# Performance work log

Hardware: AMD Instinct MI355X
Metric: run time of the kernel (lower is better)

The kernel has to match this reference:

```python
import jax, jax.numpy as jnp
import numpy as np
import itertools

# hyperparameters (match init_kwargs cfg)
V_SIZE = 32000; D = 768; H = 12; NL = 2
K_BITS = 4; L_TAB = 4; M_COPIES = 2; HID = 3072
DK = D // H; R = 1 << K_BITS; EPS = 1e-6; RMS_EPS = 1e-5

def _protos_T():
    # corners of the {-1,+1}^K hypercube, transposed -> [K, R]
    corners = np.array(list(itertools.product([-1.0, 1.0], repeat=K_BITS)), dtype=np.float32)
    return jnp.asarray(corners.T)

def setup_inputs() -> dict:
    key = jax.random.key(0)
    ks = jax.random.split(key, 14)
    s = 0.02
    return {
        "in_idx": jax.random.randint(ks[0], (1, 1024), 0, V_SIZE),
        "tok_emb": jax.random.normal(ks[1], (V_SIZE, D), jnp.float32) * s,
        "norm1_w": jnp.ones((NL, D), jnp.float32),
        "qw": jax.random.normal(ks[2], (NL, D, D), jnp.float32) * s,
        "kw": jax.random.normal(ks[3], (NL, D, D), jnp.float32) * s,
        "vw": jax.random.normal(ks[4], (NL, D, D), jnp.float32) * s,
        "ow": jax.random.normal(ks[5], (NL, D, D), jnp.float32) * s,
        "ob": jnp.zeros((NL, D), jnp.float32),
        "norm2_w": jnp.ones((NL, D), jnp.float32),
        "ff_w1": jax.random.normal(ks[6], (NL, D, HID), jnp.float32) * s,
        "ff_w2": jax.random.normal(ks[7], (NL, D, HID), jnp.float32) * s,
        "ff_w3": jax.random.normal(ks[8], (NL, HID, D), jnp.float32) * s,
        "final_norm_w": jnp.ones((D,), jnp.float32),
        "out_w": jax.random.normal(ks[9], (D, V_SIZE), jnp.float32) * s,
        "planes_T": jax.random.normal(ks[10], (NL, M_COPIES, DK, L_TAB * K_BITS), jnp.float32),
    }

def _rmsnorm(x, w):
    return x * jax.lax.rsqrt(jnp.mean(x * x, axis=-1, keepdims=True) + RMS_EPS) * w

def _race_attention(h, qw, kw, vw, ow, ob, planes, protos_T):
    B, T, _ = h.shape
    Q = (h @ qw).reshape(B, T, H, DK)
    Kt = (h @ kw).reshape(B, T, H, DK)
    Vt = (h @ vw).reshape(B, T, H, DK)
    # RoPE (split-even/odd, concat halves variant, start position 0)
    theta = 10000.0 ** (-jnp.arange(0, DK, 2, dtype=jnp.float32) / DK)
    freq = jnp.arange(T, dtype=jnp.float32)[:, None] * theta[None, :]  # [T, DK/2]
    sin = jnp.sin(freq)[None, :, None, :]
    cos = jnp.cos(freq)[None, :, None, :]
    def rope(z):
        e, o = z[..., ::2], z[..., 1::2]
        return jnp.concatenate([e * cos - o * sin, e * sin + o * cos], axis=-1)
    Q, Kt = rope(Q), rope(Kt)
    to_hb = lambda z: jnp.transpose(z, (0, 2, 1, 3)).reshape(B * H, T, DK)
    Qh, Kh, Vh = to_hb(Q), to_hb(Kt), to_hb(Vt)
    N = M_COPIES * B * H
    scale = jnp.sqrt(jnp.float32(DK))
    # random-plane projections per model copy m: [M, BH, T, L*K]
    projK = jnp.einsum('ntd,mds->mnts', Kh, planes).reshape(N, T, L_TAB, K_BITS)
    projQ = jnp.einsum('ntd,mds->mnts', Qh, planes).reshape(N, T, L_TAB, K_BITS)
    probsK = jax.nn.softmax((jnp.tanh(projK) / scale) @ protos_T, axis=-1)  # [N,T,L,R]
    probsQ = jax.nn.softmax((jnp.tanh(projQ) / scale) @ protos_T, axis=-1)
    Vn = jnp.broadcast_to(Vh[None], (M_COPIES, B * H, T, DK)).reshape(N, T, DK)
    # causal prefix sums over time
    A_pref = jnp.cumsum(probsK, axis=1)                                     # [N,T,L,R]
    B_pref = jnp.cumsum(probsK[..., None] * Vn[:, :, None, None, :], axis=1)  # [N,T,L,R,DK]
    E_pref = B_pref / (A_pref[..., None] + EPS)
    out2 = jnp.einsum('ntlr,ntlrd->ntd', probsQ, E_pref)                    # [N,T,DK]
    out_h = out2.reshape(M_COPIES, B, H, T, DK).transpose(0, 1, 3, 2, 4)    # [M,B,T,H,DK]
    m = out_h.mean(axis=0)                                                  # [B,T,H,DK]
    # faithful to the source: permute to [B,H,T,DK] then row-major reshape to [B,T,H*DK]
    out = jnp.transpose(m, (0, 2, 1, 3)).reshape(B, T, H * DK)
    return out @ ow + ob

def reference(in_idx, tok_emb, norm1_w, qw, kw, vw, ow, ob, norm2_w,
              ff_w1, ff_w2, ff_w3, final_norm_w, out_w, planes_T):
    protos_T = _protos_T()
    x = tok_emb[in_idx]  # [B,T,D]
    for l in range(NL):
        h = _rmsnorm(x, norm1_w[l])
        x = x + _race_attention(h, qw[l], kw[l], vw[l], ow[l], ob[l], planes_T[l], protos_T)
        h = _rmsnorm(x, norm2_w[l])
        x = x + (jax.nn.silu(h @ ff_w1[l]) * (h @ ff_w2[l])) @ ff_w3[l]
    x = _rmsnorm(x, final_norm_w)
    return x @ out_w  # logits [B,T,V]
```

## Files before the change

### kernel.cpp

```cpp
#include <hip/hip_runtime.h>
#include <hip/hip_bf16.h>

#define T_SEQ 1024
#define D_MODEL 768
#define QKVW 2304
#define NHEAD 12
#define NLAYER 2
#define MCOPY 2
#define HID_DIM 3072
#define VSIZE 32000
#define NCH 32
#define TL 32

typedef __attribute__((ext_vector_type(8))) short short8;
typedef __attribute__((ext_vector_type(4))) float f32x4;

__device__ __forceinline__ short f2bf(float f) {
  unsigned u = __builtin_bit_cast(unsigned, f);
  u = (u + 0x7FFFu + ((u >> 16) & 1u)) >> 16;
  return (short)u;
}

__global__ __launch_bounds__(64) void stc_k(float* __restrict__ stc) {
  int t = blockIdx.x;
  int i = threadIdx.x;
  if (i < 32) {
    float theta = powf(10000.0f, -(float)i / 32.0f);
    float s, c;
    sincosf((float)t * theta, &s, &c);
    stc[t * 64 + 2 * i] = c;
    stc[t * 64 + 2 * i + 1] = s;
  }
}

__global__ __launch_bounds__(256) void embed_k(const int* __restrict__ idx,
                                               const float* __restrict__ emb,
                                               float* __restrict__ x) {
  int t = blockIdx.x;
  int r = idx[t];
  for (int d = threadIdx.x; d < D_MODEL; d += 256)
    x[t * D_MODEL + d] = emb[r * D_MODEL + d];
}

__global__ __launch_bounds__(256) void add_norm_k(float* __restrict__ x,
                                                  const float* __restrict__ parts,
                                                  int nparts,
                                                  const float* __restrict__ bias,
                                                  const float* __restrict__ w,
                                                  short* __restrict__ out) {
  int t = blockIdx.x, tid = threadIdx.x;
  float v[3];
  float ss = 0.f;
  #pragma unroll
  for (int j = 0; j < 3; ++j) {
    int i = tid + j * 256;
    float val = x[(size_t)t * D_MODEL + i];
    if (bias) val += bias[i];
    for (int p = 0; p < nparts; ++p)
      val += parts[(size_t)p * (T_SEQ * D_MODEL) + (size_t)t * D_MODEL + i];
    v[j] = val;
    ss += val * val;
  }
  __shared__ float red[256];
  red[tid] = ss; __syncthreads();
  for (int s = 128; s > 0; s >>= 1) {
    if (tid < s) red[tid] += red[tid + s];
    __syncthreads();
  }
  float inv = rsqrtf(red[0] / (float)D_MODEL + 1e-5f);
  #pragma unroll
  for (int j = 0; j < 3; ++j) {
    int i = tid + j * 256;
    if (nparts || bias) x[(size_t)t * D_MODEL + i] = v[j];
    out[(size_t)t * D_MODEL + i] = f2bf(v[j] * inv * w[i]);
  }
}

__device__ __forceinline__ void tr_tile(const float* __restrict__ W,
                                        short* __restrict__ WT, int K, int N,
                                        int n0, int k0, int tx, int ty) {
  __shared__ float tile[32][33];
  #pragma unroll
  for (int i = 0; i < 4; ++i)
    tile[ty + 8 * i][tx] = W[(size_t)(k0 + ty + 8 * i) * N + n0 + tx];
  __syncthreads();
  #pragma unroll
  for (int i = 0; i < 4; ++i)
    WT[(size_t)(n0 + ty + 8 * i) * K + k0 + tx] = f2bf(tile[tx][ty + 8 * i]);
}

#define SQ_W  ((size_t)D_MODEL * D_MODEL)
#define FF_W  ((size_t)D_MODEL * HID_DIM)
#define LAYER_W (4 * SQ_W + 3 * FF_W)

__global__ __launch_bounds__(256) void transpose_sq8(const float* __restrict__ qw,
                                                     const float* __restrict__ kw,
                                                     const float* __restrict__ vw,
                                                     const float* __restrict__ ow,
                                                     short* __restrict__ WB) {
  int z = blockIdx.z, layer = z >> 2, which = z & 3;
  const float* W = (which == 0) ? qw : (which == 1) ? kw : (which == 2) ? vw : ow;
  W += (size_t)layer * SQ_W;
  short* WT = WB + (size_t)layer * LAYER_W + (size_t)which * SQ_W;
  tr_tile(W, WT, D_MODEL, D_MODEL, blockIdx.x * 32, blockIdx.y * 32,
          threadIdx.x, threadIdx.y);
}

__global__ __launch_bounds__(256) void transpose_ff12(const float* __restrict__ W1g,
                                                      const float* __restrict__ W2g,
                                                      short* __restrict__ WB) {
  __shared__ float tile[32][33];
  int layer = blockIdx.z;
  const float* W1 = W1g + (size_t)layer * FF_W;
  const float* W2 = W2g + (size_t)layer * FF_W;
  short* WT = WB + (size_t)layer * LAYER_W + 4 * SQ_W;
  int tx = threadIdx.x, ty = threadIdx.y;
  int n0 = blockIdx.x * 32, k0 = blockIdx.y * 32;
  int h0 = n0 >> 1;
  const float* src = (tx < 16) ? (W1 + h0 + tx) : (W2 + h0 + (tx - 16));
  #pragma unroll
  for (int i = 0; i < 4; ++i)
    tile[ty + 8 * i][tx] = src[(size_t)(k0 + ty + 8 * i) * HID_DIM];
  __syncthreads();
  #pragma unroll
  for (int i = 0; i < 4; ++i) {
    int n = ty + 8 * i;
    WT[(size_t)(n0 + n) * D_MODEL + k0 + tx] = f2bf(tile[tx][n]);
  }
}

__global__ __launch_bounds__(256) void transpose_f3(const float* __restrict__ W3g,
                                                    short* __restrict__ WB) {
  int layer = blockIdx.z;
  const float* W = W3g + (size_t)layer * FF_W;
  short* WT = WB + (size_t)layer * LAYER_W + 4 * SQ_W + 2 * FF_W;
  tr_tile(W, WT, HID_DIM, D_MODEL, blockIdx.x * 32, blockIdx.y * 32,
          threadIdx.x, threadIdx.y);
}

__global__ __launch_bounds__(256) void transpose_head(const float* __restrict__ W,
                                                      short* __restrict__ WT) {
  tr_tile(W, WT, D_MODEL, VSIZE, blockIdx.x * 32, blockIdx.y * 32,
          threadIdx.x, threadIdx.y);
}

__device__ __forceinline__ void stage_tile(const short* __restrict__ gbase,
                                           int ldK, short* lds, int tid) {
  #pragma unroll
  for (int j = 0; j < 4; ++j) {
    int r = j * 32 + (tid >> 3);
    int s = tid & 7;
    const short* gp = gbase + (size_t)r * ldK + (((s ^ (r & 7))) << 3);
    short* lp = lds + j * 2048 + tid * 8;
    __builtin_amdgcn_global_load_lds((const __attribute__((address_space(1))) void*)gp,
                                     (__attribute__((address_space(3))) void*)lp,
                                     16, 0, 0);
  }
}

__device__ __forceinline__ short8 frag_ld(const short* lds, int row, int sl) {
  return *(const short8*)(lds + row * 64 + ((sl ^ (row & 7)) << 3));
}

template<int MODE>
__global__ __launch_bounds__(256) void gemm_t(const short* __restrict__ A,
                                              const short* __restrict__ Bt,
                                              float* __restrict__ Cf,
                                              short* __restrict__ Cs,
                                              int N, int K) {
  __shared__ short As[128 * 64];
  __shared__ short Bs[128 * 64];
  int tid = threadIdx.x;
  int lane = tid & 63;
  int wave = tid >> 6;
  int wr = wave >> 1, wc = wave & 1;
  int l15 = lane & 15, kg = lane >> 4;

  int cpx = gridDim.x >> 3;
  int wg = (blockIdx.x & 7) * cpx + (blockIdx.x >> 3);
  int row0 = (wg & 7) * 128;
  int col0 = (wg >> 3) * 128;

  int kn = K / gridDim.y;
  int koff = blockIdx.y * kn;
  const short* Ab = A + (size_t)row0 * K + koff;
  const short* Bb = Bt + (size_t)col0 * K + koff;
  int nt = kn >> 6;

  f32x4 acc[4][4] = {};

  for (int t = 0; t < nt; ++t) {
    stage_tile(Ab + t * 64, K, As, tid);
    stage_tile(Bb + t * 64, K, Bs, tid);
    __syncthreads();
    #pragma unroll
    for (int kk = 0; kk < 2; ++kk) {
      short8 af[4], bf4[4];
      #pragma unroll
      for (int m = 0; m < 4; ++m)
        af[m] = frag_ld(As, wr * 64 + m * 16 + l15, 4 * kk + kg);
      #pragma unroll
      for (int n = 0; n < 4; ++n)
        bf4[n] = frag_ld(Bs, wc * 64 + n * 16 + l15, 4 * kk + kg);
      #pragma unroll
      for (int m = 0; m < 4; ++m)
        #pragma unroll
        for (int n = 0; n < 4; ++n)
          acc[m][n] = __builtin_amdgcn_mfma_f32_16x16x32_bf16(af[m], bf4[n], acc[m][n], 0, 0, 0);
    }
    __syncthreads();
  }

  int rbase = (lane >> 4) * 4;
  if constexpr (MODE == 2) {
    int base = col0 + wc * 64;
    #pragma unroll
    for (int p = 0; p < 2; ++p) {
      int h = (base >> 1) + p * 16 + l15;
      #pragma unroll
      for (int m = 0; m < 4; ++m) {
        #pragma unroll
        for (int r = 0; r < 4; ++r) {
          int row = row0 + wr * 64 + m * 16 + rbase + r;
          float g1 = acc[m][2 * p][r];
          float g2 = acc[m][2 * p + 1][r];
          Cs[(size_t)row * HID_DIM + h] = f2bf((g1 / (1.f + expf(-g1))) * g2);
        }
      }
    }
  } else {
    float* Co = Cf;
    if constexpr (MODE == 1) Co += (size_t)blockIdx.y * T_SEQ * N;
    #pragma unroll
    for (int n = 0; n < 4; ++n) {
      int col = col0 + wc * 64 + n * 16 + l15;
      #pragma unroll
      for (int m = 0; m < 4; ++m) {
        #pragma unroll
        for (int r = 0; r < 4; ++r) {
          int row = row0 + wr * 64 + m * 16 + rbase + r;
          Co[(size_t)row * N + col] = acc[m][n][r];
        }
      }
    }
  }
}

__global__ __launch_bounds__(256) void race_probs(const float* __restrict__ qkv,
                                                  const float* __restrict__ stc,
                                                  const float* __restrict__ planes,
                                                  float* __restrict__ pq,
                                                  float* __restrict__ pk) {
  int gid = blockIdx.x * 256 + threadIdx.x;
  int w = gid & 1;
  int l = (gid >> 1) & 3;
  int t = (gid >> 3) & 1023;
  int mn = gid >> 13;
  int m = mn / NHEAD, n = mn % NHEAD;
  const float* raw = qkv + (size_t)t * QKVW + (w ? 0 : D_MODEL) + n * 64;
  const float* sc = stc + t * 64;
  const float* pl = planes + m * 64 * 16 + l * 4;
  float p0 = 0.f, p1 = 0.f, p2 = 0.f, p3 = 0.f;
  #pragma unroll 4
  for (int i = 0; i < 32; ++i) {
    float e = raw[2 * i], o = raw[2 * i + 1];
    float c = sc[2 * i], s = sc[2 * i + 1];
    float re = e * c - o * s;
    float ro = e * s + o * c;
    const float* pe = pl + i * 16;
    const float* po = pl + (i + 32) * 16;
    p0 += re * pe[0] + ro * po[0];
    p1 += re * pe[1] + ro * po[1];
    p2 += re * pe[2] + ro * po[2];
    p3 += re * pe[3] + ro * po[3];
  }
  float t0 = tanhf(p0) * 0.125f;
  float t1 = tanhf(p1) * 0.125f;
  float t2 = tanhf(p2) * 0.125f;
  float t3 = tanhf(p3) * 0.125f;
  float lg[16];
  float mx = -1e30f;
  #pragma unroll
  for (int r = 0; r < 16; ++r) {
    float s = ((r & 8) ? t0 : -t0) + ((r & 4) ? t1 : -t1) +
              ((r & 2) ? t2 : -t2) + ((r & 1) ? t3 : -t3);
    lg[r] = s;
    mx = fmaxf(mx, s);
  }
  float sum = 0.f;
  #pragma unroll
  for (int r = 0; r < 16; ++r) {
    float e = expf(lg[r] - mx);
    lg[r] = e;
    sum += e;
  }
  float inv = 1.f / sum;
  float* dst = (w ? pq : pk) + ((size_t)mn * T_SEQ + t) * 64 + l * 16;
  #pragma unroll
  for (int r = 0; r < 16; ++r) dst[r] = lg[r] * inv;
}

__global__ __launch_bounds__(256) void race_chunksum(const float* __restrict__ pk_g,
                                                     const float* __restrict__ v_g,
                                                     float* __restrict__ csA,
                                                     float* __restrict__ csB) {
  int mn = blockIdx.x, ch = blockIdx.y;
  int n = mn % NHEAD;
  int tid = threadIdx.x;
  int d = tid & 63, g = tid >> 6;
  __shared__ float pk[64], vv[64];
  float a[16], bp[16];
  #pragma unroll
  for (int i = 0; i < 16; ++i) { a[i] = 0.f; bp[i] = 0.f; }
  const float* pkrow = pk_g + ((size_t)mn * T_SEQ + (size_t)ch * TL) * 64;
  const float* vrow = v_g + (size_t)(ch * TL) * QKVW + n * 64;
  for (int t = 0; t < TL; ++t) {
    if (tid < 64) pk[tid] = pkrow[t * 64 + tid];
    else if (tid < 128) vv[tid - 64] = vrow[(size_t)t * QKVW + tid - 64];
    __syncthreads();
    float vd = vv[d];
    #pragma unroll
    for (int i = 0; i < 16; ++i) {
      float p = pk[g * 16 + i];
      a[i] += p;
      bp[i] = fmaf(p, vd, bp[i]);
    }
    __syncthreads();
  }
  size_t base = ((size_t)mn * NCH + ch) * 64;
  if (d == 0) {
    #pragma unroll
    for (int i = 0; i < 16; ++i) csA[base + g * 16 + i] = a[i];
  }
  #pragma unroll
  for (int i = 0; i < 16; ++i) csB[(base + g * 16 + i) * 64 + d] = bp[i];
}

__global__ __launch_bounds__(64) void race_chunkscan(float* __restrict__ csA,
                                                     float* __restrict__ csB) {
  int mn = blockIdx.x, lr = blockIdx.y;
  int d = threadIdx.x;
  float runB = 0.f, runA = 0.f;
  for (int c = 0; c < NCH; ++c) {
    size_t ib = (((size_t)mn * NCH + c) * 64 + lr) * 64 + d;
    float b = csB[ib];
    csB[ib] = runB;
    runB += b;
    if (d == 0) {
      size_t ia = ((size_t)mn * NCH + c) * 64 + lr;
      float av = csA[ia];
      csA[ia] = runA;
      runA += av;
    }
  }
}

__global__ __launch_bounds__(256) void race_scan_emit(const float* __restrict__ pk_g,
                                                      const float* __restrict__ pq_g,
                                                      const float* __restrict__ v_g,
                                                      const float* __restrict__ csA,
                                                      const float* __restrict__ csB,
                                                      short* __restrict__ ro) {
  int n = blockIdx.x, ch = blockIdx.y;
  int tid = threadIdx.x;
  int d = tid & 63, g = tid >> 6;
  int mn0 = n, mn1 = NHEAD + n;
  __shared__ float pk0[64], pk1[64], pq0[64], pq1[64], vv[64];
  __shared__ float part[4][64];
  float a0[16], b0[16], a1[16], b1[16];
  size_t base0 = ((size_t)mn0 * NCH + ch) * 64;
  size_t base1 = ((size_t)mn1 * NCH + ch) * 64;
  #pragma unroll
  for (int i = 0; i < 16; ++i) {
    a0[i] = csA[base0 + g * 16 + i];
    b0[i] = csB[(base0 + g * 16 + i) * 64 + d];
    a1[i] = csA[base1 + g * 16 + i];
    b1[i] = csB[(base1 + g * 16 + i) * 64 + d];
  }
  const float* pk0r = pk_g + ((size_t)mn0 * T_SEQ + (size_t)ch * TL) * 64;
  const float* pk1r = pk_g + ((size_t)mn1 * T_SEQ + (size_t)ch * TL) * 64;
  const float* pq0r = pq_g + ((size_t)mn0 * T_SEQ + (size_t)ch * TL) * 64;
  const float* pq1r = pq_g + ((size_t)mn1 * T_SEQ + (size_t)ch * TL) * 64;
  const float* vrow = v_g + (size_t)(ch * TL) * QKVW + n * 64;
  for (int t = 0; t < TL; ++t) {
    if (g == 0) { pk0[d] = pk0r[t * 64 + d]; vv[d] = vrow[(size_t)t * QKVW + d]; }
    else if (g == 1) pk1[d] = pk1r[t * 64 + d];
    else if (g == 2) pq0[d] = pq0r[t * 64 + d];
    else pq1[d] = pq1r[t * 64 + d];
    __syncthreads();
    float vd = vv[d];
    float c = 0.f;
    #pragma unroll
    for (int i = 0; i < 16; ++i) {
      int lr = g * 16 + i;
      float p = pk0[lr];
      a0[i] += p;
      b0[i] = fmaf(p, vd, b0[i]);
      c = fmaf(pq0[lr] * b0[i], __builtin_amdgcn_rcpf(a0[i] + 1e-6f), c);
      p = pk1[lr];
      a1[i] += p;
      b1[i] = fmaf(p, vd, b1[i]);
      c = fmaf(pq1[lr] * b1[i], __builtin_amdgcn_rcpf(a1[i] + 1e-6f), c);
    }
    part[g][d] = c;
    __syncthreads();
    if (tid < 64) {
      float s = part[0][tid] + part[1][tid] + part[2][tid] + part[3][tid];
      ro[n * (T_SEQ * 64) + (ch * TL + t) * 64 + tid] = f2bf(0.5f * s);
    }
  }
}

extern "C" void kernel_launch(void* const* d_in, const int* in_sizes, int n_in,
                              void* d_out, int out_size, void* d_ws, size_t ws_size,
                              hipStream_t stream) {
  const int*   in_idx       = (const int*)d_in[0];
  const float* tok_emb      = (const float*)d_in[1];
  const float* norm1_w      = (const float*)d_in[2];
  const float* qw           = (const float*)d_in[3];
  const float* kw           = (const float*)d_in[4];
  const float* vw           = (const float*)d_in[5];
  const float* ow           = (const float*)d_in[6];
  const float* ob           = (const float*)d_in[7];
  const float* norm2_w      = (const float*)d_in[8];
  const float* ff_w1        = (const float*)d_in[9];
  const float* ff_w2        = (const float*)d_in[10];
  const float* ff_w3        = (const float*)d_in[11];
  const float* final_norm_w = (const float*)d_in[12];
  const float* out_w        = (const float*)d_in[13];
  const float* planes       = (const float*)d_in[14];

  float* ws = (float*)d_ws;
  const size_t SZ_TD = (size_t)T_SEQ * D_MODEL;
  float* X   = ws;
  float* STC = X + SZ_TD;
  float* S   = STC + 65536;
  short* HbB = (short*)S;
  float* QKV = S + 393216;
  float* PK  = QKV + (size_t)T_SEQ * QKVW;
  float* PQ  = PK + (size_t)MCOPY * NHEAD * T_SEQ * 64;
  float* CSA = PQ + (size_t)MCOPY * NHEAD * T_SEQ * 64;
  float* CSB = CSA + (size_t)MCOPY * NHEAD * NCH * 64;
  short* ROb = (short*)(CSB + (size_t)MCOPY * NHEAD * NCH * 64 * 64);
  short* G1B = (short*)QKV;
  float* PP  = PK;
  short* WB = (short*)(S + 9486336);
  short* outT = WB + NLAYER * LAYER_W;

  stc_k<<<T_SEQ, 64, 0, stream>>>(STC);
  dim3 tb(32, 8);
  transpose_sq8<<<dim3(24, 24, 8), tb, 0, stream>>>(qw, kw, vw, ow, WB);
  transpose_ff12<<<dim3(192, 24, 2), tb, 0, stream>>>(ff_w1, ff_w2, WB);
  transpose_f3<<<dim3(24, 96, 2), tb, 0, stream>>>(ff_w3, WB);
  transpose_head<<<dim3(1000, 24), tb, 0, stream>>>(out_w, outT);

  embed_k<<<T_SEQ, 256, 0, stream>>>(in_idx, tok_emb, X);
  add_norm_k<<<T_SEQ, 256, 0, stream>>>(X, nullptr, 0, nullptr, norm1_w, HbB);

  for (int l = 0; l < NLAYER; ++l) {
    short* base = WB + (size_t)l * LAYER_W;
    short* qkvT = base;
    short* owT  = base + 3 * SQ_W;
    short* f12T = base + 4 * SQ_W;
    short* f3T  = base + 4 * SQ_W + 2 * FF_W;

    gemm_t<0><<<dim3(8 * (QKVW / 128), 1), 256, 0, stream>>>(HbB, qkvT, QKV, nullptr, QKVW, D_MODEL);
    race_probs<<<(MCOPY * NHEAD * T_SEQ * 4 * 2) / 256, 256, 0, stream>>>(
        QKV, STC, planes + (size_t)l * MCOPY * 64 * 16, PQ, PK);
    dim3 gps(MCOPY * NHEAD, NCH);
    race_chunksum<<<gps, 256, 0, stream>>>(PK, QKV + 2 * D_MODEL, CSA, CSB);
    dim3 gcs(MCOPY * NHEAD, 64);
    race_chunkscan<<<gcs, 64, 0, stream>>>(CSA, CSB);
    dim3 gemit(NHEAD, NCH);
    race_scan_emit<<<gemit, 256, 0, stream>>>(PK, PQ, QKV + 2 * D_MODEL, CSA, CSB, ROb);
    gemm_t<1><<<dim3(8 * (D_MODEL / 128), 2), 256, 0, stream>>>(ROb, owT, PP, nullptr, D_MODEL, D_MODEL);
    add_norm_k<<<T_SEQ, 256, 0, stream>>>(X, PP, 2, ob + l * D_MODEL, norm2_w + l * D_MODEL, HbB);
    gemm_t<2><<<dim3(8 * (2 * HID_DIM / 128), 1), 256, 0, stream>>>(HbB, f12T, nullptr, G1B, 2 * HID_DIM, D_MODEL);
    gemm_t<1><<<dim3(8 * (D_MODEL / 128), 4), 256, 0, stream>>>(G1B, f3T, PP, nullptr, D_MODEL, HID_DIM);
    const float* nw = (l == NLAYER - 1) ? final_norm_w : norm1_w + (l + 1) * D_MODEL;
    add_norm_k<<<T_SEQ, 256, 0, stream>>>(X, PP, 4, nullptr, nw, HbB);
  }
  gemm_t<0><<<dim3(8 * (VSIZE / 128), 1), 256, 0, stream>>>(HbB, outT, (float*)d_out, nullptr, VSIZE, D_MODEL);
}
```

Baseline: 505.5 us.

## Double-buffer GEMM LDS tiles and fuse embedding with first RMSNorm

```diff
diff --git a/kernel.cpp b/kernel.cpp
--- a/kernel.cpp
+++ b/kernel.cpp
@@ -33,13 +33,35 @@
   }
 }
 
-__global__ __launch_bounds__(256) void embed_k(const int* __restrict__ idx,
-                                               const float* __restrict__ emb,
-                                               float* __restrict__ x) {
-  int t = blockIdx.x;
+__global__ __launch_bounds__(256) void embed_norm_k(const int* __restrict__ idx,
+                                                    const float* __restrict__ emb,
+                                                    const float* __restrict__ w,
+                                                    float* __restrict__ x,
+                                                    short* __restrict__ out) {
+  int t = blockIdx.x, tid = threadIdx.x;
   int r = idx[t];
-  for (int d = threadIdx.x; d < D_MODEL; d += 256)
-    x[t * D_MODEL + d] = emb[r * D_MODEL + d];
+  float v[3];
+  float ss = 0.f;
+  #pragma unroll
+  for (int j = 0; j < 3; ++j) {
+    int i = tid + j * 256;
+    float val = emb[(size_t)r * D_MODEL + i];
+    x[(size_t)t * D_MODEL + i] = val;
+    v[j] = val;
+    ss += val * val;
+  }
+  __shared__ float red[256];
+  red[tid] = ss; __syncthreads();
+  for (int s = 128; s > 0; s >>= 1) {
+    if (tid < s) red[tid] += red[tid + s];
+    __syncthreads();
+  }
+  float inv = rsqrtf(red[0] / (float)D_MODEL + 1e-5f);
+  #pragma unroll
+  for (int j = 0; j < 3; ++j) {
+    int i = tid + j * 256;
+    out[(size_t)t * D_MODEL + i] = f2bf(v[j] * inv * w[i]);
+  }
 }
 
 __global__ __launch_bounds__(256) void add_norm_k(float* __restrict__ x,
@@ -168,8 +190,8 @@
                                               float* __restrict__ Cf,
                                               short* __restrict__ Cs,
                                               int N, int K) {
-  __shared__ short As[128 * 64];
-  __shared__ short Bs[128 * 64];
+  __shared__ short As[2][128 * 64];
+  __shared__ short Bs[2][128 * 64];
   int tid = threadIdx.x;
   int lane = tid & 63;
   int wave = tid >> 6;
@@ -189,19 +211,27 @@
 
   f32x4 acc[4][4] = {};
 
+  stage_tile(Ab, K, As[0], tid);
+  stage_tile(Bb, K, Bs[0], tid);
+  __syncthreads();
+
+  int cur = 0;
   for (int t = 0; t < nt; ++t) {
-    stage_tile(Ab + t * 64, K, As, tid);
-    stage_tile(Bb + t * 64, K, Bs, tid);
-    __syncthreads();
+    if (t + 1 < nt) {
+      stage_tile(Ab + (t + 1) * 64, K, As[cur ^ 1], tid);
+      stage_tile(Bb + (t + 1) * 64, K, Bs[cur ^ 1], tid);
+    }
+    const short* Ac = As[cur];
+    const short* Bc = Bs[cur];
     #pragma unroll
     for (int kk = 0; kk < 2; ++kk) {
       short8 af[4], bf4[4];
       #pragma unroll
       for (int m = 0; m < 4; ++m)
-        af[m] = frag_ld(As, wr * 64 + m * 16 + l15, 4 * kk + kg);
+        af[m] = frag_ld(Ac, wr * 64 + m * 16 + l15, 4 * kk + kg);
       #pragma unroll
       for (int n = 0; n < 4; ++n)
-        bf4[n] = frag_ld(Bs, wc * 64 + n * 16 + l15, 4 * kk + kg);
+        bf4[n] = frag_ld(Bc, wc * 64 + n * 16 + l15, 4 * kk + kg);
       #pragma unroll
       for (int m = 0; m < 4; ++m)
         #pragma unroll
@@ -209,6 +239,7 @@
           acc[m][n] = __builtin_amdgcn_mfma_f32_16x16x32_bf16(af[m], bf4[n], acc[m][n], 0, 0, 0);
     }
     __syncthreads();
+    cur ^= 1;
   }
 
   int rbase = (lane >> 4) * 4;
@@ -454,8 +485,7 @@
   transpose_f3<<<dim3(24, 96, 2), tb, 0, stream>>>(ff_w3, WB);
   transpose_head<<<dim3(1000, 24), tb, 0, stream>>>(out_w, outT);
 
-  embed_k<<<T_SEQ, 256, 0, stream>>>(in_idx, tok_emb, X);
-  add_norm_k<<<T_SEQ, 256, 0, stream>>>(X, nullptr, 0, nullptr, norm1_w, HbB);
+  embed_norm_k<<<T_SEQ, 256, 0, stream>>>(in_idx, tok_emb, norm1_w, X, HbB);
 
   for (int l = 0; l < NLAYER; ++l) {
     short* base = WB + (size_t)l * LAYER_W;
```

After: 497.8 us. No clear change (-1.5%).
